# Kernel tuning notes

Measured on AMD Instinct MI355X. Metric: run time of the kernel, lower is better.

The kernel has to match this reference:

```python
import jax, jax.numpy as jnp
import numpy as np

N_NODES = 100000
N_EDGES = 1600000
IN_FEATS = 128
HEADS = 4
OUT_FEATS = 32
NEG_SLOPE = 0.2


def setup_inputs() -> dict:
    key = jax.random.key(0)
    k1, k2, k3, k4, k5, k6 = jax.random.split(key, 6)
    feat = jax.random.normal(k1, (N_NODES, IN_FEATS), dtype=jnp.float32)
    # nn.Linear(in_feats, out_feats*num_heads).weight -> [H*D_out, D_in]
    W = jax.random.normal(k2, (HEADS * OUT_FEATS, IN_FEATS), dtype=jnp.float32) * (1.0 / np.sqrt(IN_FEATS))
    attn_l = jax.random.normal(k3, (1, HEADS, OUT_FEATS), dtype=jnp.float32) * 0.1
    attn_r = jax.random.normal(k4, (1, HEADS, OUT_FEATS), dtype=jnp.float32) * 0.1
    src = jax.random.randint(k5, (N_EDGES,), 0, N_NODES, dtype=jnp.int32)
    dst = jax.random.randint(k6, (N_EDGES,), 0, N_NODES, dtype=jnp.int32)
    return {"feat": feat, "W": W, "attn_l": attn_l, "attn_r": attn_r, "src": src, "dst": dst}


def reference(feat, W, attn_l, attn_r, src, dst):
    N = feat.shape[0]
    H, D = attn_l.shape[1], attn_l.shape[2]
    # fc: feat @ W.T -> [N, H, D]
    ft = (feat @ W.T).reshape(N, H, D)
    el = jnp.sum(ft * attn_l, axis=-1)  # [N, H]
    er = jnp.sum(ft * attn_r, axis=-1)  # [N, H]
    # SDDMM edge scores (u_add_v) + leaky relu
    e = el[src] + er[dst]  # [E, H]
    e = jnp.where(e > 0, e, NEG_SLOPE * e)
    # segment softmax over edges grouped by destination node
    emax = jax.ops.segment_max(e, dst, num_segments=N)  # [N, H]
    ez = jnp.exp(e - emax[dst])
    esum = jax.ops.segment_sum(ez, dst, num_segments=N)  # [N, H]
    a = ez / esum[dst]  # [E, H]
    # weighted SpMM aggregation (u_mul_e + sum by dst)
    out = jax.ops.segment_sum(ft[src] * a[:, :, None], dst, num_segments=N)  # [N, H, D]
    return out
```

## Files before the change

kernel.cpp:

```cpp
#include <hip/hip_runtime.h>
#include <hip/hip_fp16.h>

#define IN_FEATS 128
#define HEADS 4
#define D_OUT 32
#define HD 128
#define NEG_SLOPE 0.2f

#define BSHIFT 6
#define BSIZE 64
#define CAP 1280
#define NBMAX 1600

typedef _Float16 half8 __attribute__((ext_vector_type(8)));
typedef _Float16 half4v __attribute__((ext_vector_type(4)));
typedef float floatx4 __attribute__((ext_vector_type(4)));

#define LSTR 40
#define OSTR 136
#define SMEM_BYTES (128 * OSTR * 2)

#define MAXCHUNK 3200

__global__ void init_cursor(int* __restrict__ bcursor, int NB) {
    int b = blockIdx.x * blockDim.x + threadIdx.x;
    if (b < NB) bcursor[b] = b * CAP;
}

__global__ __launch_bounds__(256) void mega(const float* __restrict__ feat,
                                            const float* __restrict__ W,
                                            const float* __restrict__ al,
                                            const float* __restrict__ ar,
                                            const int* __restrict__ src,
                                            const int* __restrict__ dst,
                                            __half* __restrict__ ft_h,
                                            float* __restrict__ el,
                                            float* __restrict__ er,
                                            int* __restrict__ bcursor,
                                            int* __restrict__ bedge,
                                            int N, int E, int NB,
                                            int gemmBlocks, int chunk) {
    __shared__ __align__(16) char smem[SMEM_BYTES];
    const int t = threadIdx.x;

    if (blockIdx.x >= gemmBlocks) {
        int* cnt = (int*)smem;
        int* base = cnt + NBMAX;
        int bid = blockIdx.x - gemmBlocks;
        int e0 = bid * chunk;
        if (e0 >= E) return;
        int e1 = e0 + chunk; if (e1 > E) e1 = E;
        int ne = e1 - e0;
        for (int b = t; b < NB; b += 256) cnt[b] = 0;
        __syncthreads();
        for (int i = t; i < ne; i += 256)
            atomicAdd(&cnt[dst[e0 + i] >> BSHIFT], 1);
        __syncthreads();
        for (int b = t; b < NB; b += 256) {
            int c = cnt[b];
            base[b] = c ? atomicAdd(&bcursor[b], c) : 0;
        }
        __syncthreads();
        for (int b = t; b < NB; b += 256) cnt[b] = 0;
        __syncthreads();
        for (int i = t; i < ne; i += 256) {
            int d = dst[e0 + i];
            int b = d >> BSHIFT;
            int p = base[b] + atomicAdd(&cnt[b], 1);
            if (p < (b + 1) * CAP)
                bedge[p] = src[e0 + i] | ((d & (BSIZE - 1)) << 17);
        }
        return;
    }

    _Float16* sh = (_Float16*)smem;
    _Float16* Als = sh;
    _Float16* Wls = sh + 5120;
    const int w = t >> 6, lane = t & 63, quad = lane >> 4, l15 = lane & 15;
    const int nodeBase = blockIdx.x * 128;

    floatx4 acc[2][8] = {};

    for (int kk = 0; kk < 4; ++kk) {
        const int k0 = kk * 32;
#pragma unroll
        for (int i = 0; i < 4; ++i) {
            int idx = i * 256 + t;
            int row = idx >> 3;
            int q = idx & 7;
            int node = nodeBase + row;
            float4 v = make_float4(0.f, 0.f, 0.f, 0.f);
            if (node < N) v = *(const float4*)(feat + (size_t)node * IN_FEATS + k0 + q * 4);
            half4v hv = {(_Float16)v.x, (_Float16)v.y, (_Float16)v.z, (_Float16)v.w};
            *(half4v*)&Als[row * LSTR + q * 4] = hv;
            float4 wv = *(const float4*)(W + (size_t)row * IN_FEATS + k0 + q * 4);
            half4v hw = {(_Float16)wv.x, (_Float16)wv.y, (_Float16)wv.z, (_Float16)wv.w};
            *(half4v*)&Wls[row * LSTR + q * 4] = hw;
        }
        __syncthreads();
        half8 af0 = *(half8*)&Als[(w * 32 + l15) * LSTR + quad * 8];
        half8 af1 = *(half8*)&Als[(w * 32 + 16 + l15) * LSTR + quad * 8];
        half8 bf[8];
#pragma unroll
        for (int nt = 0; nt < 8; ++nt)
            bf[nt] = *(half8*)&Wls[(nt * 16 + l15) * LSTR + quad * 8];
#pragma unroll
        for (int nt = 0; nt < 8; ++nt) {
            acc[0][nt] = __builtin_amdgcn_mfma_f32_16x16x32_f16(af0, bf[nt], acc[0][nt], 0, 0, 0);
            acc[1][nt] = __builtin_amdgcn_mfma_f32_16x16x32_f16(af1, bf[nt], acc[1][nt], 0, 0, 0);
        }
        __syncthreads();
    }

#pragma unroll
    for (int mt = 0; mt < 2; ++mt)
#pragma unroll
        for (int nt = 0; nt < 8; ++nt)
#pragma unroll
            for (int r = 0; r < 4; ++r)
                sh[(w * 32 + mt * 16 + quad * 4 + r) * OSTR + nt * 16 + l15] =
                    (_Float16)acc[mt][nt][r];
    __syncthreads();

    const int row = t >> 1, seg = t & 1;
    const int node = nodeBase + row;
    half8 hv[8];
#pragma unroll
    for (int j = 0; j < 8; ++j) hv[j] = *(half8*)&sh[row * OSTR + seg * 64 + j * 8];

    float accl0 = 0.f, accl1 = 0.f, accr0 = 0.f, accr1 = 0.f;
#pragma unroll
    for (int j = 0; j < 8; ++j) {
        float4 a0 = *(const float4*)(al + seg * 64 + j * 8);
        float4 a1 = *(const float4*)(al + seg * 64 + j * 8 + 4);
        float4 r0 = *(const float4*)(ar + seg * 64 + j * 8);
        float4 r1 = *(const float4*)(ar + seg * 64 + j * 8 + 4);
        float v0 = (float)hv[j][0], v1 = (float)hv[j][1], v2 = (float)hv[j][2], v3 = (float)hv[j][3];
        float v4 = (float)hv[j][4], v5 = (float)hv[j][5], v6 = (float)hv[j][6], v7 = (float)hv[j][7];
        float dl = v0 * a0.x + v1 * a0.y + v2 * a0.z + v3 * a0.w
                 + v4 * a1.x + v5 * a1.y + v6 * a1.z + v7 * a1.w;
        float dr = v0 * r0.x + v1 * r0.y + v2 * r0.z + v3 * r0.w
                 + v4 * r1.x + v5 * r1.y + v6 * r1.z + v7 * r1.w;
        if (j < 4) { accl0 += dl; accr0 += dr; }
        else       { accl1 += dl; accr1 += dr; }
    }
    if (node < N) {
#pragma unroll
        for (int j = 0; j < 8; ++j)
            *(half8*)(ft_h + (size_t)node * HD + seg * 64 + j * 8) = hv[j];
        el[node * 4 + seg * 2 + 0] = accl0;
        el[node * 4 + seg * 2 + 1] = accl1;
        er[node * 4 + seg * 2 + 0] = accr0;
        er[node * 4 + seg * 2 + 1] = accr1;
    }
}

__global__ __launch_bounds__(256) void bucket_aggregate(const __half* __restrict__ ft_h,
                                                        const float* __restrict__ el,
                                                        const float* __restrict__ er,
                                                        const int* __restrict__ bcursor,
                                                        const int* __restrict__ bedge,
                                                        float* __restrict__ out, int N) {
    __shared__ int eS[CAP];
    __shared__ uint2 eW[CAP];
    __shared__ float4 er4L[BSIZE];
    __shared__ int cnt[BSIZE];
    __shared__ int exs[BSIZE];
    __shared__ int pos[BSIZE];
    const int b = blockIdx.x, t = threadIdx.x;
    const int s0 = b * CAP;
    const int node0 = b << BSHIFT;
    int cntE = bcursor[b] - s0;
    if (cntE > CAP) cntE = CAP;
    if (t < BSIZE) {
        cnt[t] = 0;
        int n = node0 + t;
        er4L[t] = (n < N) ? *(const float4*)(er + (size_t)n * 4)
                          : make_float4(0.f, 0.f, 0.f, 0.f);
    }
    __syncthreads();
    for (int i = t; i < cntE; i += 256)
        atomicAdd(&cnt[bedge[s0 + i] >> 17], 1);
    __syncthreads();
    if (t < BSIZE) {
        int x = cnt[t];
        int inc = x;
#pragma unroll
        for (int off = 1; off < 64; off <<= 1) {
            int y = __shfl_up(inc, off);
            if (t >= off) inc += y;
        }
        exs[t] = inc - x;
        pos[t] = inc - x;
    }
    __syncthreads();
    for (int i = t; i < cntE; i += 256) {
        int v = bedge[s0 + i];
        int dl = v >> 17;
        int s = v & 0x1FFFF;
        float4 el4 = *(const float4*)(el + (size_t)s * 4);
        float4 e4 = er4L[dl];
        float x0 = el4.x + e4.x; x0 = x0 > 0.f ? x0 : NEG_SLOPE * x0;
        float x1 = el4.y + e4.y; x1 = x1 > 0.f ? x1 : NEG_SLOPE * x1;
        float x2 = el4.z + e4.z; x2 = x2 > 0.f ? x2 : NEG_SLOPE * x2;
        float x3 = el4.w + e4.w; x3 = x3 > 0.f ? x3 : NEG_SLOPE * x3;
        __half2 p01 = __floats2half2_rn(__expf(x0), __expf(x1));
        __half2 p23 = __floats2half2_rn(__expf(x2), __expf(x3));
        uint2 pk;
        pk.x = *(unsigned int*)&p01;
        pk.y = *(unsigned int*)&p23;
        int p = atomicAdd(&pos[dl], 1);
        eS[p] = s;
        eW[p] = pk;
    }
    __syncthreads();

    const int wid = t >> 6, lane = t & 63;
    const int g = lane >> 4;
    const int q = lane & 15;
    const int h = q >> 2;
    const unsigned short* eWu = (const unsigned short*)eW;

    for (int dl = wid; dl < BSIZE; dl += 4) {
        int n = node0 + dl;
        if (n >= N) break;
        int start = exs[dl];
        int end = start + cnt[dl];

        float a0 = 0.f, a1 = 0.f, a2 = 0.f, a3 = 0.f;
        float a4 = 0.f, a5 = 0.f, a6 = 0.f, a7 = 0.f;
        float ws = 0.f;

        for (int bb = start; bb < end; bb += 8) {
            int e0 = bb + g;
            int e1 = e0 + 4;
            bool v0 = e0 < end, v1 = e1 < end;
            int sA = v0 ? eS[e0] : 0;
            int sB = v1 ? eS[e1] : 0;
            unsigned short uA = v0 ? eWu[e0 * 4 + h] : (unsigned short)0;
            unsigned short uB = v1 ? eWu[e1 * 4 + h] : (unsigned short)0;
            int4 rawA = *(const int4*)(ft_h + (size_t)sA * HD + q * 8);
            int4 rawB = *(const int4*)(ft_h + (size_t)sB * HD + q * 8);
            float w0 = v0 ? __half2float(*(__half*)&uA) : 0.f;
            float w1 = v1 ? __half2float(*(__half*)&uB) : 0.f;
            float2 fA0 = __half22float2(*(__half2*)&rawA.x);
            float2 fA1 = __half22float2(*(__half2*)&rawA.y);
            float2 fA2 = __half22float2(*(__half2*)&rawA.z);
            float2 fA3 = __half22float2(*(__half2*)&rawA.w);
            float2 fB0 = __half22float2(*(__half2*)&rawB.x);
            float2 fB1 = __half22float2(*(__half2*)&rawB.y);
            float2 fB2 = __half22float2(*(__half2*)&rawB.z);
            float2 fB3 = __half22float2(*(__half2*)&rawB.w);
            a0 += w0 * fA0.x + w1 * fB0.x;  a1 += w0 * fA0.y + w1 * fB0.y;
            a2 += w0 * fA1.x + w1 * fB1.x;  a3 += w0 * fA1.y + w1 * fB1.y;
            a4 += w0 * fA2.x + w1 * fB2.x;  a5 += w0 * fA2.y + w1 * fB2.y;
            a6 += w0 * fA3.x + w1 * fB3.x;  a7 += w0 * fA3.y + w1 * fB3.y;
            ws += w0 + w1;
        }
        a0 += __shfl_xor(a0, 16); a0 += __shfl_xor(a0, 32);
        a1 += __shfl_xor(a1, 16); a1 += __shfl_xor(a1, 32);
        a2 += __shfl_xor(a2, 16); a2 += __shfl_xor(a2, 32);
        a3 += __shfl_xor(a3, 16); a3 += __shfl_xor(a3, 32);
        a4 += __shfl_xor(a4, 16); a4 += __shfl_xor(a4, 32);
        a5 += __shfl_xor(a5, 16); a5 += __shfl_xor(a5, 32);
        a6 += __shfl_xor(a6, 16); a6 += __shfl_xor(a6, 32);
        a7 += __shfl_xor(a7, 16); a7 += __shfl_xor(a7, 32);
        ws += __shfl_xor(ws, 16); ws += __shfl_xor(ws, 32);
        float inv = ws > 0.f ? 1.0f / ws : 0.f;
        float r0 = (g == 0 ? a0 : g == 1 ? a2 : g == 2 ? a4 : a6) * inv;
        float r1 = (g == 0 ? a1 : g == 1 ? a3 : g == 2 ? a5 : a7) * inv;
        *(float2*)(out + (size_t)n * HD + q * 8 + g * 2) = make_float2(r0, r1);
    }
}

extern "C" void kernel_launch(void* const* d_in, const int* in_sizes, int n_in,
                              void* d_out, int out_size, void* d_ws, size_t ws_size,
                              hipStream_t stream) {
    const float* feat = (const float*)d_in[0];
    const float* W    = (const float*)d_in[1];
    const float* al   = (const float*)d_in[2];
    const float* ar   = (const float*)d_in[3];
    const int* src    = (const int*)d_in[4];
    const int* dst    = (const int*)d_in[5];
    float* out        = (float*)d_out;

    const int N = in_sizes[0] / IN_FEATS;
    const int E = in_sizes[4];
    const int NB = (N + BSIZE - 1) >> BSHIFT;

    char* ws = (char*)d_ws;
    size_t off = 0;
    auto alloc = [&](size_t bytes) {
        void* p = ws + off;
        off += (bytes + 255) & ~(size_t)255;
        return p;
    };
    __half* ft_h   = (__half*)alloc((size_t)N * HD * 2);
    float* el      = (float*)alloc((size_t)N * 4 * 4);
    float* er      = (float*)alloc((size_t)N * 4 * 4);
    int*   bcursor = (int*)alloc((size_t)NBMAX * 4);
    int*   bedge   = (int*)alloc((size_t)NB * CAP * 4);
    (void)ws_size;

    init_cursor<<<(NB + 255) / 256, 256, 0, stream>>>(bcursor, NB);
    int gemmBlocks = (N + 127) / 128;
    int grid2 = 512;
    int chunk = (E + grid2 - 1) / grid2;
    if (chunk > MAXCHUNK) chunk = MAXCHUNK;
    int nblk = (E + chunk - 1) / chunk;
    mega<<<gemmBlocks + nblk, 256, 0, stream>>>(feat, W, al, ar, src, dst,
                                                ft_h, el, er, bcursor, bedge,
                                                N, E, NB, gemmBlocks, chunk);
    bucket_aggregate<<<NB, 256, 0, stream>>>(ft_h, el, er, bcursor, bedge, out, N);
}
```

Before: 245.2 us.

## Replace atomic bucket cursors with deterministic histogram, scan, scatter passes

Splits edge bucketing into three passes: a per-chunk histogram kernel, a column scan fused into the GEMM launch that computes per-chunk write offsets and bucket totals, and a separate scatter kernel. This replaces the global atomicAdd on shared bucket cursors and gives each chunk contiguous, deterministic slots within each bucket. It adds two kernel launches, extra reads of dst, and hist/base arrays of 256×NB ints each. The scatter can no longer overlap with the GEMM blocks.

```diff
diff --git a/kernel.cpp b/kernel.cpp
--- a/kernel.cpp
+++ b/kernel.cpp
@@ -12,6 +12,9 @@
 #define CAP 1280
 #define NBMAX 1600
 
+#define G_SCAT 256
+#define SCAN_BK 64
+
 typedef _Float16 half8 __attribute__((ext_vector_type(8)));
 typedef _Float16 half4v __attribute__((ext_vector_type(4)));
 typedef float floatx4 __attribute__((ext_vector_type(4)));
@@ -20,55 +23,63 @@
 #define OSTR 136
 #define SMEM_BYTES (128 * OSTR * 2)
 
-#define MAXCHUNK 3200
-
-__global__ void init_cursor(int* __restrict__ bcursor, int NB) {
-    int b = blockIdx.x * blockDim.x + threadIdx.x;
-    if (b < NB) bcursor[b] = b * CAP;
+__global__ __launch_bounds__(256) void hist_kernel(const int* __restrict__ dst,
+                                                   int* __restrict__ hist,
+                                                   int E, int NB, int chunk) {
+    __shared__ int cnt[NBMAX];
+    const int t = threadIdx.x;
+    const int g = blockIdx.x;
+    int e0 = g * chunk;
+    int e1 = e0 + chunk; if (e1 > E) e1 = E;
+    for (int b = t; b < NB; b += 256) cnt[b] = 0;
+    __syncthreads();
+    for (int i = e0 + t; i < e1; i += 256)
+        atomicAdd(&cnt[dst[i] >> BSHIFT], 1);
+    __syncthreads();
+    for (int b = t; b < NB; b += 256)
+        hist[(size_t)g * NB + b] = cnt[b];
 }
 
 __global__ __launch_bounds__(256) void mega(const float* __restrict__ feat,
                                             const float* __restrict__ W,
                                             const float* __restrict__ al,
                                             const float* __restrict__ ar,
-                                            const int* __restrict__ src,
-                                            const int* __restrict__ dst,
                                             __half* __restrict__ ft_h,
                                             float* __restrict__ el,
                                             float* __restrict__ er,
-                                            int* __restrict__ bcursor,
-                                            int* __restrict__ bedge,
-                                            int N, int E, int NB,
-                                            int gemmBlocks, int chunk) {
+                                            const int* __restrict__ hist,
+                                            int* __restrict__ base,
+                                            int* __restrict__ total,
+                                            int N, int NB, int gemmBlocks) {
     __shared__ __align__(16) char smem[SMEM_BYTES];
     const int t = threadIdx.x;
 
     if (blockIdx.x >= gemmBlocks) {
-        int* cnt = (int*)smem;
-        int* base = cnt + NBMAX;
-        int bid = blockIdx.x - gemmBlocks;
-        int e0 = bid * chunk;
-        if (e0 >= E) return;
-        int e1 = e0 + chunk; if (e1 > E) e1 = E;
-        int ne = e1 - e0;
-        for (int b = t; b < NB; b += 256) cnt[b] = 0;
+        int* psum = (int*)smem;
+        const int sb = blockIdx.x - gemmBlocks;
+        const int tb = t & 63, tg = t >> 6;
+        const int b = sb * SCAN_BK + tb;
+        const bool valid = b < NB;
+        int s = 0;
+        if (valid) {
+#pragma unroll 8
+            for (int j = 0; j < G_SCAT / 4; ++j)
+                s += hist[(size_t)(tg * (G_SCAT / 4) + j) * NB + b];
+        }
+        psum[tg * 64 + tb] = s;
         __syncthreads();
-        for (int i = t; i < ne; i += 256)
-            atomicAdd(&cnt[dst[e0 + i] >> BSHIFT], 1);
-        __syncthreads();
-        for (int b = t; b < NB; b += 256) {
-            int c = cnt[b];
-            base[b] = c ? atomicAdd(&bcursor[b], c) : 0;
-        }
-        __syncthreads();
-        for (int b = t; b < NB; b += 256) cnt[b] = 0;
-        __syncthreads();
-        for (int i = t; i < ne; i += 256) {
-            int d = dst[e0 + i];
-            int b = d >> BSHIFT;
-            int p = base[b] + atomicAdd(&cnt[b], 1);
-            if (p < (b + 1) * CAP)
-                bedge[p] = src[e0 + i] | ((d & (BSIZE - 1)) << 17);
+        int ex = 0;
+        for (int u = 0; u < tg; ++u) ex += psum[u * 64 + tb];
+        if (valid) {
+            if (tg == 3) total[b] = ex + s;
+            int run = b * CAP + ex;
+#pragma unroll 8
+            for (int j = 0; j < G_SCAT / 4; ++j) {
+                size_t idx = (size_t)(tg * (G_SCAT / 4) + j) * NB + b;
+                int v = hist[idx];
+                base[idx] = run;
+                run += v;
+            }
         }
         return;
     }
@@ -155,10 +166,35 @@
     }
 }
 
+__global__ __launch_bounds__(256) void scatter_kernel(const int* __restrict__ src,
+                                                      const int* __restrict__ dst,
+                                                      const int* __restrict__ base,
+                                                      int* __restrict__ bedge,
+                                                      int E, int NB, int chunk) {
+    __shared__ int cnt[NBMAX];
+    __shared__ int bl[NBMAX];
+    const int t = threadIdx.x;
+    const int g = blockIdx.x;
+    int e0 = g * chunk;
+    int e1 = e0 + chunk; if (e1 > E) e1 = E;
+    for (int b = t; b < NB; b += 256) {
+        cnt[b] = 0;
+        bl[b] = base[(size_t)g * NB + b];
+    }
+    __syncthreads();
+    for (int i = e0 + t; i < e1; i += 256) {
+        int d = dst[i];
+        int b = d >> BSHIFT;
+        int p = bl[b] + atomicAdd(&cnt[b], 1);
+        if (p < (b + 1) * CAP)
+            bedge[p] = src[i] | ((d & (BSIZE - 1)) << 17);
+    }
+}
+
 __global__ __launch_bounds__(256) void bucket_aggregate(const __half* __restrict__ ft_h,
                                                         const float* __restrict__ el,
                                                         const float* __restrict__ er,
-                                                        const int* __restrict__ bcursor,
+                                                        const int* __restrict__ total,
                                                         const int* __restrict__ bedge,
                                                         float* __restrict__ out, int N) {
     __shared__ int eS[CAP];
@@ -170,7 +206,7 @@
     const int b = blockIdx.x, t = threadIdx.x;
     const int s0 = b * CAP;
     const int node0 = b << BSHIFT;
-    int cntE = bcursor[b] - s0;
+    int cntE = total[b];
     if (cntE > CAP) cntE = CAP;
     if (t < BSIZE) {
         cnt[t] = 0;
@@ -295,21 +331,24 @@
         off += (bytes + 255) & ~(size_t)255;
         return p;
     };
-    __half* ft_h   = (__half*)alloc((size_t)N * HD * 2);
-    float* el      = (float*)alloc((size_t)N * 4 * 4);
-    float* er      = (float*)alloc((size_t)N * 4 * 4);
-    int*   bcursor = (int*)alloc((size_t)NBMAX * 4);
-    int*   bedge   = (int*)alloc((size_t)NB * CAP * 4);
+    __half* ft_h  = (__half*)alloc((size_t)N * HD * 2);
+    float* el     = (float*)alloc((size_t)N * 4 * 4);
+    float* er     = (float*)alloc((size_t)N * 4 * 4);
+    int*   hist   = (int*)alloc((size_t)G_SCAT * NB * 4);
+    int*   base   = (int*)alloc((size_t)G_SCAT * NB * 4);
+    int*   total  = (int*)alloc((size_t)NBMAX * 4);
+    int*   bedge  = (int*)alloc((size_t)NB * CAP * 4);
     (void)ws_size;
 
-    init_cursor<<<(NB + 255) / 256, 256, 0, stream>>>(bcursor, NB);
-    int gemmBlocks = (N + 127) / 128;
-    int grid2 = 512;
-    int chunk = (E + grid2 - 1) / grid2;
-    if (chunk > MAXCHUNK) chunk = MAXCHUNK;
-    int nblk = (E + chunk - 1) / chunk;
-    mega<<<gemmBlocks + nblk, 256, 0, stream>>>(feat, W, al, ar, src, dst,
-                                                ft_h, el, er, bcursor, bedge,
-                                                N, E, NB, gemmBlocks, chunk);
-    bucket_aggregate<<<NB, 256, 0, stream>>>(ft_h, el, er, bcursor, bedge, out, N);
-}
+    const int chunk = (E + G_SCAT - 1) / G_SCAT;
+
+    hist_kernel<<<G_SCAT, 256, 0, stream>>>(dst, hist, E, NB, chunk);
+    const int gemmBlocks = (N + 127) / 128;
+    const int scanBlocks = (NB + SCAN_BK - 1) / SCAN_BK;
+    mega<<<gemmBlocks + scanBlocks, 256, 0, stream>>>(feat, W, al, ar,
+                                                      ft_h, el, er,
+                                                      hist, base, total,
+                                                      N, NB, gemmBlocks);
+    scatter_kernel<<<G_SCAT, 256, 0, stream>>>(src, dst, base, bedge, E, NB, chunk);
+    bucket_aggregate<<<NB, 256, 0, stream>>>(ft_h, el, er, total, bedge, out, N);
+}
```

Measured after the change: 263.3 us. 7.4% more time.

## Assign one destination node per 16-lane group and unroll edge gathers by eight

Applied to the files above, without the earlier changes.

The aggregation loop now gives each 16-lane quarter of a wavefront its own destination node, so a wave handles four nodes at once instead of splitting one node's edges across lane groups. This removes the cross-group shuffle reduction and the select-based output write, and each lane now writes eight outputs with float4 stores. Within a node, eight edge gathers are issued before any accumulation to expose more memory-level parallelism. The cost is more registers per lane and possible load imbalance between groups with different degrees, which also causes divergence inside the wave.

```diff
diff --git a/kernel.cpp b/kernel.cpp
--- a/kernel.cpp
+++ b/kernel.cpp
@@ -12,6 +12,9 @@
 #define CAP 1280
 #define NBMAX 1600
 
+#define BSCAT 6
+#define MAXCHUNK 3200
+
 typedef _Float16 half8 __attribute__((ext_vector_type(8)));
 typedef _Float16 half4v __attribute__((ext_vector_type(4)));
 typedef float floatx4 __attribute__((ext_vector_type(4)));
@@ -19,8 +22,6 @@
 #define LSTR 40
 #define OSTR 136
 #define SMEM_BYTES (128 * OSTR * 2)
-
-#define MAXCHUNK 3200
 
 __global__ void init_cursor(int* __restrict__ bcursor, int NB) {
     int b = blockIdx.x * blockDim.x + threadIdx.x;
@@ -221,55 +222,50 @@
     const int h = q >> 2;
     const unsigned short* eWu = (const unsigned short*)eW;
 
-    for (int dl = wid; dl < BSIZE; dl += 4) {
+    for (int dl = wid * 4 + g; dl < BSIZE; dl += 16) {
         int n = node0 + dl;
-        if (n >= N) break;
-        int start = exs[dl];
-        int end = start + cnt[dl];
+        const bool alive = n < N;
+        int start = alive ? exs[dl] : 0;
+        int end = alive ? start + cnt[dl] : 0;
 
         float a0 = 0.f, a1 = 0.f, a2 = 0.f, a3 = 0.f;
         float a4 = 0.f, a5 = 0.f, a6 = 0.f, a7 = 0.f;
         float ws = 0.f;
 
         for (int bb = start; bb < end; bb += 8) {
-            int e0 = bb + g;
-            int e1 = e0 + 4;
-            bool v0 = e0 < end, v1 = e1 < end;
-            int sA = v0 ? eS[e0] : 0;
-            int sB = v1 ? eS[e1] : 0;
-            unsigned short uA = v0 ? eWu[e0 * 4 + h] : (unsigned short)0;
-            unsigned short uB = v1 ? eWu[e1 * 4 + h] : (unsigned short)0;
-            int4 rawA = *(const int4*)(ft_h + (size_t)sA * HD + q * 8);
-            int4 rawB = *(const int4*)(ft_h + (size_t)sB * HD + q * 8);
-            float w0 = v0 ? __half2float(*(__half*)&uA) : 0.f;
-            float w1 = v1 ? __half2float(*(__half*)&uB) : 0.f;
-            float2 fA0 = __half22float2(*(__half2*)&rawA.x);
-            float2 fA1 = __half22float2(*(__half2*)&rawA.y);
-            float2 fA2 = __half22float2(*(__half2*)&rawA.z);
-            float2 fA3 = __half22float2(*(__half2*)&rawA.w);
-            float2 fB0 = __half22float2(*(__half2*)&rawB.x);
-            float2 fB1 = __half22float2(*(__half2*)&rawB.y);
-            float2 fB2 = __half22float2(*(__half2*)&rawB.z);
-            float2 fB3 = __half22float2(*(__half2*)&rawB.w);
-            a0 += w0 * fA0.x + w1 * fB0.x;  a1 += w0 * fA0.y + w1 * fB0.y;
-            a2 += w0 * fA1.x + w1 * fB1.x;  a3 += w0 * fA1.y + w1 * fB1.y;
-            a4 += w0 * fA2.x + w1 * fB2.x;  a5 += w0 * fA2.y + w1 * fB2.y;
-            a6 += w0 * fA3.x + w1 * fB3.x;  a7 += w0 * fA3.y + w1 * fB3.y;
-            ws += w0 + w1;
-        }
-        a0 += __shfl_xor(a0, 16); a0 += __shfl_xor(a0, 32);
-        a1 += __shfl_xor(a1, 16); a1 += __shfl_xor(a1, 32);
-        a2 += __shfl_xor(a2, 16); a2 += __shfl_xor(a2, 32);
-        a3 += __shfl_xor(a3, 16); a3 += __shfl_xor(a3, 32);
-        a4 += __shfl_xor(a4, 16); a4 += __shfl_xor(a4, 32);
-        a5 += __shfl_xor(a5, 16); a5 += __shfl_xor(a5, 32);
-        a6 += __shfl_xor(a6, 16); a6 += __shfl_xor(a6, 32);
-        a7 += __shfl_xor(a7, 16); a7 += __shfl_xor(a7, 32);
-        ws += __shfl_xor(ws, 16); ws += __shfl_xor(ws, 32);
+            int4 raw[8];
+            float wv[8];
+#pragma unroll
+            for (int j = 0; j < 8; ++j) {
+                int e = bb + j;
+                bool v = e < end;
+                int s = v ? eS[e] : 0;
+                unsigned short u = v ? eWu[e * 4 + h] : (unsigned short)0;
+                raw[j] = *(const int4*)(ft_h + (size_t)s * HD + q * 8);
+                wv[j] = v ? __half2float(*(__half*)&u) : 0.f;
+            }
+#pragma unroll
+            for (int j = 0; j < 8; ++j) {
+                float2 f0 = __half22float2(*(__half2*)&raw[j].x);
+                float2 f1 = __half22float2(*(__half2*)&raw[j].y);
+                float2 f2 = __half22float2(*(__half2*)&raw[j].z);
+                float2 f3 = __half22float2(*(__half2*)&raw[j].w);
+                float w0 = wv[j];
+                a0 += w0 * f0.x;  a1 += w0 * f0.y;
+                a2 += w0 * f1.x;  a3 += w0 * f1.y;
+                a4 += w0 * f2.x;  a5 += w0 * f2.y;
+                a6 += w0 * f3.x;  a7 += w0 * f3.y;
+                ws += w0;
+            }
+        }
         float inv = ws > 0.f ? 1.0f / ws : 0.f;
-        float r0 = (g == 0 ? a0 : g == 1 ? a2 : g == 2 ? a4 : a6) * inv;
-        float r1 = (g == 0 ? a1 : g == 1 ? a3 : g == 2 ? a5 : a7) * inv;
-        *(float2*)(out + (size_t)n * HD + q * 8 + g * 2) = make_float2(r0, r1);
+        if (alive) {
+            float4 o0 = make_float4(a0 * inv, a1 * inv, a2 * inv, a3 * inv);
+            float4 o1 = make_float4(a4 * inv, a5 * inv, a6 * inv, a7 * inv);
+            float* op = out + (size_t)n * HD + q * 8;
+            *(float4*)op = o0;
+            *(float4*)(op + 4) = o1;
+        }
     }
 }
 
```

Result: no change. 249.4 us (+1.7%).
